# Kernel tuning notes

Hardware: AMD Instinct MI355X
Metric: run time of the kernel (lower is better)

## Reference

```python
import jax, jax.numpy as jnp
import numpy as np

N = 100000      # number of nodes
E = 1600000     # number of (directed) edges, avg degree 16
DIN = 128       # in_features
DOUT = 32       # out_features
SLOPE = 0.2     # leaky relu negative slope


def setup_inputs() -> dict:
    key = jax.random.key(0)
    k1, k2, k3, k4, k5, k6 = jax.random.split(key, 6)
    x = jax.random.normal(k1, (N, DIN), dtype=jnp.float32)
    edge_index = jax.random.randint(k2, (2, E), 0, N, dtype=jnp.int32)
    # W1 (shared with W2 and used as the feature-update matrix W, 'source' mode)
    W1_w = jax.random.normal(k3, (DOUT, DIN), dtype=jnp.float32) / np.float32(np.sqrt(DIN))
    W1_b = jax.random.normal(k4, (DOUT,), dtype=jnp.float32) * 0.01
    a1_w = jax.random.normal(k5, (DOUT,), dtype=jnp.float32) / np.float32(np.sqrt(DOUT))
    a2_w = jax.random.normal(k6, (DOUT,), dtype=jnp.float32) / np.float32(np.sqrt(DOUT))
    return {"x": x, "edge_index": edge_index, "W1_w": W1_w, "W1_b": W1_b,
            "a1_w": a1_w, "a2_w": a2_w}


def reference(x, edge_index, W1_w, W1_b, a1_w, a2_w):
    n = x.shape[0]
    # append self-loops, as in _sparse_attention
    loops = jnp.arange(n, dtype=edge_index.dtype)
    src = jnp.concatenate([edge_index[0], loops])   # rows  (softmax segments)
    dst = jnp.concatenate([edge_index[1], loops])   # cols
    # h = W1(x) (linear, with bias); W2 = W1 (weight sharing), W = W2 ('source')
    h = x @ W1_w.T + W1_b                           # [N, DOUT]
    z = jax.nn.leaky_relu(h, SLOPE)                 # x1 == x2 under weight sharing
    s1 = z @ a1_w                                   # [N] per-node src score
    s2 = z @ a2_w                                   # [N] per-node dst score
    logits = s1[src] + s2[dst]                      # [E+N] per-edge attention logit
    # row-wise (dim=1) sparse softmax == segment softmax over src
    m = jax.ops.segment_max(logits, src, num_segments=n)
    ex = jnp.exp(logits - m[src])
    denom = jax.ops.segment_sum(ex, src, num_segments=n)
    alpha = ex / denom[src]                         # normalized attention per edge
    # sparse-dense matmul: out[i] = sum_{(i,j)} alpha_ij * h[j]
    return jax.ops.segment_sum(alpha[:, None] * h[dst], src, num_segments=n)
```

## Files before the change

kernel.cpp:

```cpp
#include <hip/hip_runtime.h>
#include <hip/hip_fp16.h>

#define DIN 128
#define DOUT 32
#define SLOPE 0.2f

#define BSHIFT 7
#define BNODES 128
#define NBS    1024
#define CAP    3072
#define TILE   4096
#define EPB    (TILE / 256)
#define TPW    4

typedef short s16x8 __attribute__((ext_vector_type(8)));
typedef float f32x4 __attribute__((ext_vector_type(4)));

__device__ __forceinline__ short f2bf(float f) {
    unsigned u = __float_as_uint(f);
    return (short)((u + 0x7fffu + ((u >> 16) & 1u)) >> 16);
}
__device__ __forceinline__ float bf2f(short s) {
    return __uint_as_float(((unsigned)(unsigned short)s) << 16);
}

__device__ __forceinline__ void linear_role(
    int wid, int ntiles, int lane, int N,
    const float* __restrict__ x, const float* __restrict__ W,
    const float* __restrict__ b, const float* __restrict__ a2,
    __half* __restrict__ g16, float* __restrict__ es2)
{
    if (wid * TPW >= ntiles) return;
    int m = lane & 15, oct = lane >> 4;

    s16x8 bh[2][4], bl[2][4];
    #pragma unroll
    for (int t = 0; t < 2; ++t) {
        const float* wrow = W + (long)(t * 16 + m) * DIN + oct * 8;
        #pragma unroll
        for (int kc = 0; kc < 4; ++kc) {
            float4 w0 = *(const float4*)(wrow + kc * 32);
            float4 w1 = *(const float4*)(wrow + kc * 32 + 4);
            float wf[8] = {w0.x, w0.y, w0.z, w0.w, w1.x, w1.y, w1.z, w1.w};
            #pragma unroll
            for (int j = 0; j < 8; ++j) {
                short hh = f2bf(wf[j]);
                bh[t][kc][j] = hh;
                bl[t][kc][j] = f2bf(wf[j] - bf2f(hh));
            }
        }
    }

    int c0 = m, c1 = 16 + m;
    float b0 = b[c0], b1 = b[c1], A0 = a2[c0], A1 = a2[c1];

    #pragma unroll 1
    for (int g = 0; g < TPW; ++g) {
        int tile = wid * TPW + g;
        if (tile >= ntiles) break;
        long rowbase = (long)tile * 16;

        long lrow = rowbase + m; if (lrow > N - 1) lrow = N - 1;
        const float* xrow = x + lrow * DIN + oct * 8;
        f32x4 acc0 = {0.f, 0.f, 0.f, 0.f}, acc1 = {0.f, 0.f, 0.f, 0.f};
        #pragma unroll
        for (int kc = 0; kc < 4; ++kc) {
            float4 x0 = *(const float4*)(xrow + kc * 32);
            float4 x1 = *(const float4*)(xrow + kc * 32 + 4);
            float xf[8] = {x0.x, x0.y, x0.z, x0.w, x1.x, x1.y, x1.z, x1.w};
            s16x8 ah, al;
            #pragma unroll
            for (int j = 0; j < 8; ++j) {
                short hh = f2bf(xf[j]);
                ah[j] = hh;
                al[j] = f2bf(xf[j] - bf2f(hh));
            }
            acc0 = __builtin_amdgcn_mfma_f32_16x16x32_bf16(al, bh[0][kc], acc0, 0, 0, 0);
            acc0 = __builtin_amdgcn_mfma_f32_16x16x32_bf16(ah, bl[0][kc], acc0, 0, 0, 0);
            acc0 = __builtin_amdgcn_mfma_f32_16x16x32_bf16(ah, bh[0][kc], acc0, 0, 0, 0);
            acc1 = __builtin_amdgcn_mfma_f32_16x16x32_bf16(al, bh[1][kc], acc1, 0, 0, 0);
            acc1 = __builtin_amdgcn_mfma_f32_16x16x32_bf16(ah, bl[1][kc], acc1, 0, 0, 0);
            acc1 = __builtin_amdgcn_mfma_f32_16x16x32_bf16(ah, bh[1][kc], acc1, 0, 0, 0);
        }

        float hv0[4], hv1[4], sp[4];
        #pragma unroll
        for (int i = 0; i < 4; ++i) {
            hv0[i] = acc0[i] + b0;
            hv1[i] = acc1[i] + b1;
            float z0 = hv0[i] > 0.f ? hv0[i] : SLOPE * hv0[i];
            float z1 = hv1[i] > 0.f ? hv1[i] : SLOPE * hv1[i];
            sp[i] = z0 * A0 + z1 * A1;
        }
        #pragma unroll
        for (int off = 1; off <= 8; off <<= 1) {
            #pragma unroll
            for (int i = 0; i < 4; ++i) sp[i] += __shfl_xor(sp[i], off, 64);
        }
        #pragma unroll
        for (int i = 0; i < 4; ++i) {
            long r = rowbase + oct * 4 + i;
            if (r >= N) continue;
            float ev = __expf(sp[i]);
            g16[r * DOUT + c0] = __float2half(ev * hv0[i]);
            g16[r * DOUT + c1] = __float2half(ev * hv1[i]);
            if (m == 0) es2[r] = ev;
        }
    }
}

__global__ __launch_bounds__(256) void gat_fused(
    const float* __restrict__ x, const float* __restrict__ W,
    const float* __restrict__ b, const float* __restrict__ a2,
    const int* __restrict__ src, const int* __restrict__ dst,
    __half* __restrict__ g16, float* __restrict__ es2,
    unsigned* __restrict__ ebuf, int* __restrict__ boffT,
    int N, int E, int ntiles, int nbin, int nbinp)
{
    if ((int)blockIdx.x >= nbin) {
        int wave = threadIdx.x >> 6;
        int wid = (blockIdx.x - nbin) * 4 + wave;
        linear_role(wid, ntiles, threadIdx.x & 63, N, x, W, b, a2, g16, es2);
        return;
    }
    __shared__ int cnt[NBS];
    __shared__ int offs[NBS];
    __shared__ int wsum[4], wbase[4];
    int tid = threadIdx.x;
    long tstart = (long)blockIdx.x * TILE;

    for (int i = tid; i < NBS; i += 256) cnt[i] = 0;
    __syncthreads();

    unsigned rec[EPB];
    int      bq[EPB];
    #pragma unroll
    for (int it = 0; it < EPB; ++it) {
        long e = tstart + it * 256 + tid;
        int s = (e < E) ? src[e] : -1;
        int d = (e < E) ? dst[e] : 0;
        if (s >= 0) {
            int bk = s >> BSHIFT;
            int rv = atomicAdd(&cnt[bk], 1);
            rec[it] = ((unsigned)(s & (BNODES - 1)) << 17) | (unsigned)d;
            bq[it] = (rv < 511) ? ((bk << 9) | rv) : -1;
        } else bq[it] = -1;
    }
    __syncthreads();

    int t4 = tid << 2;
    int c0 = cnt[t4], c1 = cnt[t4 + 1], c2 = cnt[t4 + 2], c3 = cnt[t4 + 3];
    int s4 = c0 + c1 + c2 + c3;
    int v = s4;
    #pragma unroll
    for (int off = 1; off < 64; off <<= 1) {
        int t = __shfl_up(v, off, 64);
        if ((tid & 63) >= off) v += t;
    }
    if ((tid & 63) == 63) wsum[tid >> 6] = v;
    __syncthreads();
    if (tid == 0) {
        int a = 0;
        #pragma unroll
        for (int w = 0; w < 4; ++w) { wbase[w] = a; a += wsum[w]; }
    }
    __syncthreads();
    int base = wbase[tid >> 6] + (v - s4);
    offs[t4]     = base;
    offs[t4 + 1] = base + c0;
    offs[t4 + 2] = base + c0 + c1;
    offs[t4 + 3] = base + c0 + c1 + c2;
    __syncthreads();

    int NBv = (N + BNODES - 1) >> BSHIFT;
    for (int i = tid; i <= NBv; i += 256)
        boffT[(size_t)i * nbinp + blockIdx.x] = offs[i];

    #pragma unroll
    for (int it = 0; it < EPB; ++it) {
        int q = bq[it];
        if (q >= 0) {
            int pos = offs[q >> 9] + (q & 511);
            ebuf[tstart + pos] = rec[it];
        }
    }
}

__global__ __launch_bounds__(512) void gat_aggregate(
    const __half* __restrict__ g16, const float* __restrict__ es2,
    const unsigned* __restrict__ ebuf, const int* __restrict__ boffT,
    float* __restrict__ out, int N, int nbin, int nbinp)
{
    __shared__ unsigned srt[CAP];
    __shared__ unsigned srca[CAP];
    __shared__ int cnt[BNODES];
    __shared__ int basep[BNODES];
    __shared__ int pos2[BNODES];
    __shared__ int wsum[8], wbase[8], totsh;
    int tid = threadIdx.x;

    int nwg = gridDim.x;
    int xcd = blockIdx.x & 7;
    int q = nwg >> 3, rr = nwg & 7;
    int bk = (xcd < rr ? xcd * (q + 1) : rr * (q + 1) + (xcd - rr) * q)
           + ((int)blockIdx.x >> 3);

    if (tid < BNODES) { cnt[tid] = 0; pos2[tid] = 0; }

    int rstart = 0, rlen = 0;
    if (tid < nbin) {
        rstart = boffT[(size_t)bk * nbinp + tid];
        rlen   = boffT[(size_t)(bk + 1) * nbinp + tid] - rstart;
    }
    int v = rlen;
    #pragma unroll
    for (int off = 1; off < 64; off <<= 1) {
        int t = __shfl_up(v, off, 64);
        if ((tid & 63) >= off) v += t;
    }
    if ((tid & 63) == 63) wsum[tid >> 6] = v;
    __syncthreads();
    if (tid == 0) {
        int a = 0;
        #pragma unroll
        for (int w = 0; w < 8; ++w) { wbase[w] = a; a += wsum[w]; }
        totsh = a;
    }
    __syncthreads();
    int dest = wbase[tid >> 6] + (v - rlen);
    int lim = CAP - dest; if (lim < 0) lim = 0;
    if (rlen > lim) rlen = lim;
    {
        unsigned abase = (unsigned)tid * TILE + (unsigned)rstart;
        for (int j = 0; j < rlen; ++j)
            srca[dest + j] = abase + (unsigned)j;
    }
    __syncthreads();
    int cntb = totsh; if (cntb > CAP) cntb = CAP;

    unsigned held[6];
    #pragma unroll
    for (int k = 0; k < 6; ++k) {
        int r = tid + (k << 9);
        held[k] = 0xFFFFFFFFu;
        if (r < cntb) held[k] = ebuf[(size_t)srca[r]];
    }
    #pragma unroll
    for (int k = 0; k < 6; ++k) {
        unsigned u = held[k];
        if (u != 0xFFFFFFFFu) atomicAdd(&cnt[u >> 17], 1);
    }
    __syncthreads();

    if (tid < 64) {
        int a = cnt[2 * tid], b2 = cnt[2 * tid + 1];
        int s = a + b2;
        int vv = s;
        #pragma unroll
        for (int off = 1; off < 64; off <<= 1) {
            int t = __shfl_up(vv, off, 64);
            if (tid >= off) vv += t;
        }
        int excl = vv - s;
        basep[2 * tid]     = excl;
        basep[2 * tid + 1] = excl + a;
    }
    __syncthreads();

    #pragma unroll
    for (int k = 0; k < 6; ++k) {
        unsigned u = held[k];
        if (u != 0xFFFFFFFFu) {
            int sl = (int)(u >> 17);
            int p = basep[sl] + atomicAdd(&pos2[sl], 1);
            srt[p] = u & 0x1FFFFu;
        }
    }
    __syncthreads();

    int unit = tid >> 5, col = tid & 31;
    for (int sl = unit; sl < BNODES; sl += 16) {
        long node = (long)bk * BNODES + sl;
        if (node >= N) break;
        float acc = __half2float(g16[node * DOUT + col]);
        float d = es2[node];
        int e = basep[sl], e_end = basep[sl] + cnt[sl];

        while (e + 8 <= e_end) {
            int dn[8];
            #pragma unroll
            for (int j = 0; j < 8; ++j) dn[j] = (int)srt[e + j];
            unsigned short gv[8];
            #pragma unroll
            for (int j = 0; j < 8; ++j)
                gv[j] = *(const unsigned short*)&g16[(long)dn[j] * DOUT + col];
            float ev[8];
            #pragma unroll
            for (int j = 0; j < 8; ++j) ev[j] = es2[dn[j]];
            #pragma unroll
            for (int j = 0; j < 8; ++j) {
                acc += __half2float(*(const __half*)&gv[j]);
                d += ev[j];
            }
            e += 8;
        }
        while (e + 4 <= e_end) {
            int dn[4];
            #pragma unroll
            for (int j = 0; j < 4; ++j) dn[j] = (int)srt[e + j];
            unsigned short gv[4];
            #pragma unroll
            for (int j = 0; j < 4; ++j)
                gv[j] = *(const unsigned short*)&g16[(long)dn[j] * DOUT + col];
            float ev[4];
            #pragma unroll
            for (int j = 0; j < 4; ++j) ev[j] = es2[dn[j]];
            #pragma unroll
            for (int j = 0; j < 4; ++j) {
                acc += __half2float(*(const __half*)&gv[j]);
                d += ev[j];
            }
            e += 4;
        }
        for (; e < e_end; ++e) {
            int dn = (int)srt[e];
            acc += __half2float(g16[(long)dn * DOUT + col]);
            d += es2[dn];
        }
        out[node * DOUT + col] = acc / d;
    }
}

extern "C" void kernel_launch(void* const* d_in, const int* in_sizes, int n_in,
                              void* d_out, int out_size, void* d_ws, size_t ws_size,
                              hipStream_t stream)
{
    const float* x  = (const float*)d_in[0];
    const int*   ei = (const int*)d_in[1];
    const float* W  = (const float*)d_in[2];
    const float* b  = (const float*)d_in[3];
    const float* a2 = (const float*)d_in[5];
    float* out = (float*)d_out;

    int N = in_sizes[0] / DIN;
    int E = in_sizes[1] / 2;
    const int* src = ei;
    const int* dst = ei + E;

    int NB = (N + BNODES - 1) >> BSHIFT;
    int nbin = (E + TILE - 1) / TILE;
    int nbinp = (nbin + 7) & ~7;

    char* ws = (char*)d_ws;
    __half*   g16   = (__half*)ws;  ws += (size_t)N * DOUT * sizeof(__half);
    float*    es2   = (float*)ws;   ws += (size_t)N * sizeof(float);
    int*      boffT = (int*)ws;     ws += (size_t)(NB + 1) * nbinp * sizeof(int);
    unsigned* ebuf  = (unsigned*)ws; ws += (size_t)nbin * TILE * sizeof(unsigned);

    int ntiles = (N + 15) / 16;
    int nwaves = (ntiles + TPW - 1) / TPW;
    int nlin   = (nwaves + 3) / 4;

    gat_fused    <<<nbin + nlin, 256, 0, stream>>>(x, W, b, a2, src, dst,
                                                   g16, es2, ebuf, boffT,
                                                   N, E, ntiles, nbin, nbinp);
    gat_aggregate<<<NB, 512, 0, stream>>>(g16, es2, ebuf, boffT, out, N,
                                          nbin, nbinp);
}
```

Before: 154.1 us.

## Prefetch x rows across tiles and spread denominator loads across lanes

In the linear role, each wave now loads half of the next tile's x row into registers while computing the current tile, so load latency overlaps with MFMA work. In the aggregate kernel, per-node edge segments in shared memory are padded to multiples of 4, which allows vectorized uint4 index loads. The per-edge es2 loads are spread across lanes and combined with a shuffle reduction instead of every lane loading all of them. This adds register pressure and extra shared memory for the padding, and the shuffle reduction adds a few instructions per node.

```diff
diff --git a/kernel.cpp b/kernel.cpp
--- a/kernel.cpp
+++ b/kernel.cpp
@@ -9,6 +9,7 @@
 #define BNODES 128
 #define NBS    1024
 #define CAP    3072
+#define SRTCAP (CAP + 384)
 #define TILE   4096
 #define EPB    (TILE / 256)
 #define TPW    4
@@ -54,19 +55,49 @@
     int c0 = m, c1 = 16 + m;
     float b0 = b[c0], b1 = b[c1], A0 = a2[c0], A1 = a2[c1];
 
+    float4 cxa[4];
+    {
+        long lrow = (long)(wid * TPW) * 16 + m; if (lrow > N - 1) lrow = N - 1;
+        const float* xrow = x + lrow * DIN + oct * 8;
+        #pragma unroll
+        for (int kc = 0; kc < 2; ++kc) {
+            cxa[2 * kc]     = *(const float4*)(xrow + kc * 32);
+            cxa[2 * kc + 1] = *(const float4*)(xrow + kc * 32 + 4);
+        }
+    }
+
     #pragma unroll 1
     for (int g = 0; g < TPW; ++g) {
         int tile = wid * TPW + g;
         if (tile >= ntiles) break;
         long rowbase = (long)tile * 16;
-
         long lrow = rowbase + m; if (lrow > N - 1) lrow = N - 1;
         const float* xrow = x + lrow * DIN + oct * 8;
+
+        float4 cxb[4];
+        #pragma unroll
+        for (int kc = 0; kc < 2; ++kc) {
+            cxb[2 * kc]     = *(const float4*)(xrow + (kc + 2) * 32);
+            cxb[2 * kc + 1] = *(const float4*)(xrow + (kc + 2) * 32 + 4);
+        }
+
+        bool hasnext = (g + 1 < TPW) && (tile + 1 < ntiles);
+        float4 nxa[4];
+        if (hasnext) {
+            long nrow = rowbase + 16 + m; if (nrow > N - 1) nrow = N - 1;
+            const float* nx = x + nrow * DIN + oct * 8;
+            #pragma unroll
+            for (int kc = 0; kc < 2; ++kc) {
+                nxa[2 * kc]     = *(const float4*)(nx + kc * 32);
+                nxa[2 * kc + 1] = *(const float4*)(nx + kc * 32 + 4);
+            }
+        }
+
         f32x4 acc0 = {0.f, 0.f, 0.f, 0.f}, acc1 = {0.f, 0.f, 0.f, 0.f};
         #pragma unroll
         for (int kc = 0; kc < 4; ++kc) {
-            float4 x0 = *(const float4*)(xrow + kc * 32);
-            float4 x1 = *(const float4*)(xrow + kc * 32 + 4);
+            float4 x0 = (kc < 2) ? cxa[2 * kc]     : cxb[2 * (kc - 2)];
+            float4 x1 = (kc < 2) ? cxa[2 * kc + 1] : cxb[2 * (kc - 2) + 1];
             float xf[8] = {x0.x, x0.y, x0.z, x0.w, x1.x, x1.y, x1.z, x1.w};
             s16x8 ah, al;
             #pragma unroll
@@ -105,6 +136,10 @@
             g16[r * DOUT + c0] = __float2half(ev * hv0[i]);
             g16[r * DOUT + c1] = __float2half(ev * hv1[i]);
             if (m == 0) es2[r] = ev;
+        }
+        if (hasnext) {
+            #pragma unroll
+            for (int i = 0; i < 4; ++i) cxa[i] = nxa[i];
         }
     }
 }
@@ -191,7 +226,7 @@
     const unsigned* __restrict__ ebuf, const int* __restrict__ boffT,
     float* __restrict__ out, int N, int nbin, int nbinp)
 {
-    __shared__ unsigned srt[CAP];
+    __shared__ unsigned srt[SRTCAP];
     __shared__ unsigned srca[CAP];
     __shared__ int cnt[BNODES];
     __shared__ int basep[BNODES];
@@ -254,7 +289,8 @@
 
     if (tid < 64) {
         int a = cnt[2 * tid], b2 = cnt[2 * tid + 1];
-        int s = a + b2;
+        int pa = (a + 3) & ~3, pb = (b2 + 3) & ~3;
+        int s = pa + pb;
         int vv = s;
         #pragma unroll
         for (int off = 1; off < 64; off <<= 1) {
@@ -263,7 +299,7 @@
         }
         int excl = vv - s;
         basep[2 * tid]     = excl;
-        basep[2 * tid + 1] = excl + a;
+        basep[2 * tid + 1] = excl + pa;
     }
     __syncthreads();
 
@@ -279,55 +315,57 @@
     __syncthreads();
 
     int unit = tid >> 5, col = tid & 31;
+    int lane64 = tid & 63;
     for (int sl = unit; sl < BNODES; sl += 16) {
         long node = (long)bk * BNODES + sl;
         if (node >= N) break;
         float acc = __half2float(g16[node * DOUT + col]);
-        float d = es2[node];
+        float selfe = es2[node];
+        float dpart = 0.f;
         int e = basep[sl], e_end = basep[sl] + cnt[sl];
 
         while (e + 8 <= e_end) {
-            int dn[8];
-            #pragma unroll
-            for (int j = 0; j < 8; ++j) dn[j] = (int)srt[e + j];
+            uint4 q0 = *(const uint4*)&srt[e];
+            uint4 q1 = *(const uint4*)&srt[e + 4];
+            float evp = 0.f;
+            if (col < 8) evp = es2[srt[e + col]];
+            int dn[8] = {(int)q0.x, (int)q0.y, (int)q0.z, (int)q0.w,
+                         (int)q1.x, (int)q1.y, (int)q1.z, (int)q1.w};
             unsigned short gv[8];
             #pragma unroll
             for (int j = 0; j < 8; ++j)
                 gv[j] = *(const unsigned short*)&g16[(long)dn[j] * DOUT + col];
-            float ev[8];
-            #pragma unroll
-            for (int j = 0; j < 8; ++j) ev[j] = es2[dn[j]];
-            #pragma unroll
-            for (int j = 0; j < 8; ++j) {
+            dpart += evp;
+            #pragma unroll
+            for (int j = 0; j < 8; ++j)
                 acc += __half2float(*(const __half*)&gv[j]);
-                d += ev[j];
-            }
             e += 8;
         }
         while (e + 4 <= e_end) {
-            int dn[4];
-            #pragma unroll
-            for (int j = 0; j < 4; ++j) dn[j] = (int)srt[e + j];
+            uint4 q0 = *(const uint4*)&srt[e];
+            float evp = 0.f;
+            if (col < 4) evp = es2[srt[e + col]];
+            int dn[4] = {(int)q0.x, (int)q0.y, (int)q0.z, (int)q0.w};
             unsigned short gv[4];
             #pragma unroll
             for (int j = 0; j < 4; ++j)
                 gv[j] = *(const unsigned short*)&g16[(long)dn[j] * DOUT + col];
-            float ev[4];
-            #pragma unroll
-            for (int j = 0; j < 4; ++j) ev[j] = es2[dn[j]];
-            #pragma unroll
-            for (int j = 0; j < 4; ++j) {
+            dpart += evp;
+            #pragma unroll
+            for (int j = 0; j < 4; ++j)
                 acc += __half2float(*(const __half*)&gv[j]);
-                d += ev[j];
-            }
             e += 4;
         }
         for (; e < e_end; ++e) {
             int dn = (int)srt[e];
             acc += __half2float(g16[(long)dn * DOUT + col]);
-            d += es2[dn];
-        }
-        out[node * DOUT + col] = acc / d;
+            if (col == 0) dpart += es2[dn];
+        }
+        #pragma unroll
+        for (int off = 1; off < 8; off <<= 1)
+            dpart += __shfl_xor(dpart, off, 64);
+        float dtot = __shfl(dpart, lane64 & 32, 64);
+        out[node * DOUT + col] = acc / (selfe + dtot);
     }
 }
 
```

Measured after the change: 155.1 us. Within noise of the previous version (+0.7%).
